# Optimization experiments

Measured on AMD Instinct MI355X. Metric: run time of the kernel, lower is better.

The kernel has to match this reference:

```python
import jax, jax.numpy as jnp
import numpy as np

B, Q, K, DQ, DK = 4, 256, 1024, 256, 256


def setup_inputs() -> dict:
    key = jax.random.key(0)
    ks = jax.random.split(key, 7)
    q = jax.random.normal(ks[0], (B, Q, DQ), dtype=jnp.float32)
    k = jax.random.normal(ks[1], (B, K, DK), dtype=jnp.float32)
    v = jax.random.normal(ks[2], (B, K, DK), dtype=jnp.float32)
    mask = jax.random.randint(ks[3], (B, K), 0, 2).astype(bool)
    # torch Linear(in,out,bias=False): y = x @ W.T ; store as [in,out] for einsum
    Wq = jax.random.normal(ks[4], (DQ, DK), dtype=jnp.float32) / np.sqrt(DQ)
    Wk = jax.random.normal(ks[5], (DK, DK), dtype=jnp.float32) / np.sqrt(DK)
    wv = jax.random.normal(ks[6], (DK,), dtype=jnp.float32) / np.sqrt(DK)
    return {"q": q, "k": k, "v": v, "mask": mask, "Wq": Wq, "Wk": Wk, "wv": wv}


def reference(q, k, v, mask, Wq, Wk, wv):
    # Additive (Bahdanau) attention. Original redundantly projects repeated
    # copies; projecting once then broadcasting is the same math.
    qp = jnp.einsum('bqd,de->bqe', q, Wq)          # [B,Q,DK]
    kp = jnp.einsum('bkd,de->bke', k, Wk)          # [B,K,DK]
    h = jnp.tanh(qp[:, :, None, :] + kp[:, None, :, :])  # [B,Q,K,DK]
    scores = jnp.einsum('bqke,e->bqk', h, wv)      # [B,Q,K]
    scores = jnp.where(mask[:, None, :], scores, -jnp.inf)
    probs = jax.nn.softmax(scores, axis=-1)        # [B,Q,K]
    attended = jnp.einsum('bqk,bkd->bqd', probs, v)
    return attended
```

## Files before the change

kernel.cpp:

```cpp
#include <hip/hip_runtime.h>
#include <hip/hip_bf16.h>

#define B_ 4
#define Q_ 256
#define K_ 1024
#define D_ 256
#define LOG2E 1.44269504f

__device__ __forceinline__ float fexp2(float x) {
    float r; asm("v_exp_f32 %0, %1" : "=v"(r) : "v"(x)); return r;
}
__device__ __forceinline__ float frcp(float x) {
    float r; asm("v_rcp_f32 %0, %1" : "=v"(r) : "v"(x)); return r;
}
__device__ __forceinline__ void gload_lds16(const void* g, void* l) {
    __builtin_amdgcn_global_load_lds((const __attribute__((address_space(1))) void*)g,
                                     (__attribute__((address_space(3))) void*)l, 16, 0, 0);
}

__global__ __launch_bounds__(256) void prep_kernel(const float* __restrict__ q,
                                                   const float* __restrict__ k,
                                                   const float* __restrict__ Wq,
                                                   const float* __restrict__ Wk,
                                                   const int* __restrict__ mask,
                                                   float* __restrict__ qpE,
                                                   float* __restrict__ kpE,
                                                   ushort* __restrict__ kidx,
                                                   int* __restrict__ nvalid,
                                                   float scale) {
    const int t = threadIdx.x;
    if (blockIdx.x >= 80) {
        if (t >= 64) return;
        const int b = blockIdx.y, lane = t;
        const int* m = mask + b * K_;
        const int base = lane * 16;
        int cnt = 0;
#pragma unroll
        for (int i = 0; i < 16; ++i) cnt += (m[base + i] != 0);
        int inc = cnt;
#pragma unroll
        for (int d = 1; d < 64; d <<= 1) {
            int tt = __shfl_up(inc, d);
            if (lane >= d) inc += tt;
        }
        const int total = __shfl(inc, 63);
        int pos = inc - cnt;
        ushort* kb = kidx + b * K_;
        for (int i = 0; i < 16; ++i) {
            int kk = base + i;
            if (m[kk] != 0) kb[pos++] = (ushort)kk;
        }
        for (int j = total + lane; j < K_; j += 64) kb[j] = 0;
        if (lane == 0) nvalid[b] = total;
        return;
    }
    const float* A; const float* W; float* outp; int m0;
    if (blockIdx.x < 16) { A = q; W = Wq; outp = qpE; m0 = blockIdx.x * 64; }
    else                 { A = k; W = Wk; outp = kpE; m0 = (blockIdx.x - 16) * 64; }
    __shared__ float As[16][65];
    __shared__ float Ws[16][64];
    const int tx = t & 15, ty = t >> 4;
    const int n0 = blockIdx.y * 64;
    const int ar = t >> 2, ac = (t & 3) * 4;
    const int wr = t >> 4, wc = (t & 15) * 4;
    float c[4][4] = {};
    for (int kb = 0; kb < 256; kb += 16) {
        __syncthreads();
        float4 av = *(const float4*)(A + (size_t)(m0 + ar) * 256 + kb + ac);
        As[ac + 0][ar] = av.x; As[ac + 1][ar] = av.y;
        As[ac + 2][ar] = av.z; As[ac + 3][ar] = av.w;
        float4 wvv = *(const float4*)(W + (size_t)(kb + wr) * 256 + n0 + wc);
        wvv.x *= scale; wvv.y *= scale; wvv.z *= scale; wvv.w *= scale;
        *(float4*)(&Ws[wr][wc]) = wvv;
        __syncthreads();
#pragma unroll
        for (int kk = 0; kk < 16; ++kk) {
            float4 bv = *(const float4*)(&Ws[kk][tx * 4]);
#pragma unroll
            for (int i = 0; i < 4; ++i) {
                float a = As[kk][ty * 4 + i];
                c[i][0] = fmaf(a, bv.x, c[i][0]);
                c[i][1] = fmaf(a, bv.y, c[i][1]);
                c[i][2] = fmaf(a, bv.z, c[i][2]);
                c[i][3] = fmaf(a, bv.w, c[i][3]);
            }
        }
    }
#pragma unroll
    for (int i = 0; i < 4; ++i) {
        float4 o = make_float4(fexp2(c[i][0]), fexp2(c[i][1]),
                               fexp2(c[i][2]), fexp2(c[i][3]));
        *(float4*)(outp + (size_t)(m0 + ty * 4 + i) * 256 + n0 + tx * 4) = o;
    }
}

__global__ __launch_bounds__(1024, 2) void attn_kernel(const float* __restrict__ qpE,
                                                       const float* __restrict__ kpE,
                                                       const float* __restrict__ v,
                                                       const ushort* __restrict__ kidx_g,
                                                       const int* __restrict__ nvalid_g,
                                                       const float* __restrict__ wv,
                                                       float* __restrict__ out) {
    __shared__ float4 s_kp[2][32 * 65];
    __shared__ float  s_red[16 * 66];
    __shared__ float  s_sc[2][1024];
    __shared__ ushort s_kidx[1024];
    __shared__ float  s_inv[2];

    const int tid  = threadIdx.x;
    const int lane = tid & 63;
    const int wave = tid >> 6;
    const int kl   = lane & 31;
    const int eh   = lane >> 5;

    int bid = blockIdx.x;
    bid = (bid & 7) * 64 + (bid >> 3);
    const int b  = bid >> 7;
    const int qi = bid & 127;
    const int q0 = qi * 2;

    const int nv     = nvalid_g[b];
    const int ntiles = (nv + 31) >> 5;
    const int ntot   = ntiles << 5;

    s_kidx[tid] = (tid < nv) ? kidx_g[b * K_ + tid] : (ushort)0;

    float qp_A[2][8], wv_r[8];
    {
        const int e0 = wave * 16 + eh * 8;
#pragma unroll
        for (int qq = 0; qq < 2; ++qq) {
            const float4* p = (const float4*)(qpE + ((size_t)(b * Q_ + q0 + qq) << 8) + e0);
#pragma unroll
            for (int i = 0; i < 2; ++i) {
                float4 x = p[i];
                qp_A[qq][i * 4 + 0] = x.x; qp_A[qq][i * 4 + 1] = x.y;
                qp_A[qq][i * 4 + 2] = x.z; qp_A[qq][i * 4 + 3] = x.w;
            }
        }
        const float4* pw = (const float4*)(wv + e0);
#pragma unroll
        for (int i = 0; i < 2; ++i) {
            float4 x = pw[i];
            wv_r[i * 4 + 0] = x.x; wv_r[i * 4 + 1] = x.y;
            wv_r[i * 4 + 2] = x.z; wv_r[i * 4 + 3] = x.w;
        }
    }
    __syncthreads();

    const float4* srcb = (const float4*)(kpE + ((size_t)b * K_ << 8));

    if (ntiles > 0) {
#pragma unroll
        for (int i = 0; i < 2; ++i) {
            const int row = wave * 2 + i;
            const int gr = s_kidx[row];
            gload_lds16(srcb + ((size_t)gr << 6) + lane, &s_kp[0][row * 65]);
        }
    }
    __syncthreads();

    for (int kt = 0; kt < ntiles; ++kt) {
        const int p = kt & 1;
        if (kt + 1 < ntiles) {
            const int o = (kt + 1) * 32;
#pragma unroll
            for (int i = 0; i < 2; ++i) {
                const int row = wave * 2 + i;
                const int gr = s_kidx[o + row];
                gload_lds16(srcb + ((size_t)gr << 6) + lane, &s_kp[p ^ 1][row * 65]);
            }
        }
        float a0 = 0.f, a1 = 0.f;
        const float4* krow = s_kp[p] + kl * 65 + wave * 4 + eh * 2;
#pragma unroll
        for (int t4 = 0; t4 < 2; ++t4) {
            float4 kv = krow[t4];
            float kc[4] = {kv.x, kv.y, kv.z, kv.w};
#pragma unroll
            for (int j = 0; j < 4; ++j) {
                const int e = t4 * 4 + j;
                const float w = wv_r[e];
                float r0 = frcp(fmaf(qp_A[0][e], kc[j], 1.0f));
                a0 = fmaf(w, r0, a0);
                float r1 = frcp(fmaf(qp_A[1][e], kc[j], 1.0f));
                a1 = fmaf(w, r1, a1);
            }
        }
        a0 += __shfl_xor(a0, 32);
        a1 += __shfl_xor(a1, 32);
        if (eh == 0) {
            s_red[wave * 66 + kl]      = a0;
            s_red[wave * 66 + 32 + kl] = a1;
        }
        __syncthreads();

        {
            const int w = tid & 15, sl = tid >> 4;
            float s = s_red[w * 66 + sl];
            s += __shfl_xor(s, 1);
            s += __shfl_xor(s, 2);
            s += __shfl_xor(s, 4);
            s += __shfl_xor(s, 8);
            if (w == 0) {
                const int idx = kt * 32 + (sl & 31);
                s_sc[sl >> 5][idx] = (idx < nv) ? (-2.0f * s) : -3.0e38f;
            }
        }
        __syncthreads();
    }

    if (wave < 2) {
        const int qq = wave;
        float mx = -3.0e38f;
        for (int j = lane; j < ntot; j += 64) mx = fmaxf(mx, s_sc[qq][j]);
#pragma unroll
        for (int off = 32; off > 0; off >>= 1) mx = fmaxf(mx, __shfl_xor(mx, off));
        float sum = 0.f;
        for (int j = lane; j < ntot; j += 64) {
            float e = fexp2((s_sc[qq][j] - mx) * LOG2E);
            s_sc[qq][j] = e;
            sum += e;
        }
#pragma unroll
        for (int off = 32; off > 0; off >>= 1) sum += __shfl_xor(sum, off);
        if (lane == 0) s_inv[qq] = frcp(sum);
    }
    __syncthreads();

    {
        const int dl = tid & 63;
        const int kq = tid >> 6;
        const int chunk = ntiles * 2;
        float4 o0 = {0, 0, 0, 0}, o1 = {0, 0, 0, 0};
        const float4* v4 = (const float4*)(v + ((size_t)b * K_ << 8));
        for (int k = kq * chunk; k < kq * chunk + chunk; ++k) {
            int vr = s_kidx[k];
            float4 vv = v4[((size_t)vr << 6) + dl];
            float p0 = s_sc[0][k], p1 = s_sc[1][k];
            o0.x = fmaf(p0, vv.x, o0.x); o0.y = fmaf(p0, vv.y, o0.y);
            o0.z = fmaf(p0, vv.z, o0.z); o0.w = fmaf(p0, vv.w, o0.w);
            o1.x = fmaf(p1, vv.x, o1.x); o1.y = fmaf(p1, vv.y, o1.y);
            o1.z = fmaf(p1, vv.z, o1.z); o1.w = fmaf(p1, vv.w, o1.w);
        }
        float4* s_pv = s_kp[0];
        s_pv[(kq * 2 + 0) * 64 + dl] = o0;
        s_pv[(kq * 2 + 1) * 64 + dl] = o1;
        __syncthreads();
        if (tid < 128) {
            const int qq = tid >> 6, c = tid & 63;
            float4 s = {0, 0, 0, 0};
#pragma unroll
            for (int g = 0; g < 16; ++g) {
                float4 x = s_pv[(g * 2 + qq) * 64 + c];
                s.x += x.x; s.y += x.y; s.z += x.z; s.w += x.w;
            }
            const float inv = s_inv[qq];
            s.x *= inv; s.y *= inv; s.z *= inv; s.w *= inv;
            ((float4*)out)[((size_t)(b * Q_ + q0 + qq) << 6) + c] = s;
        }
    }
}

extern "C" void kernel_launch(void* const* d_in, const int* in_sizes, int n_in,
                              void* d_out, int out_size, void* d_ws, size_t ws_size,
                              hipStream_t stream) {
    const float* q    = (const float*)d_in[0];
    const float* k    = (const float*)d_in[1];
    const float* v    = (const float*)d_in[2];
    const int*   mask = (const int*)d_in[3];
    const float* Wq   = (const float*)d_in[4];
    const float* Wk   = (const float*)d_in[5];
    const float* wv   = (const float*)d_in[6];
    float* out = (float*)d_out;

    float* qpE    = (float*)d_ws;
    float* kpE    = qpE + (size_t)B_ * Q_ * D_;
    ushort* kidx  = (ushort*)(kpE + (size_t)B_ * K_ * D_);
    int* nvalid   = (int*)(kidx + (size_t)B_ * K_);

    const float c2 = 2.885390082f;

    prep_kernel<<<dim3(81, 4), 256, 0, stream>>>(q, k, Wq, Wk, mask, qpE, kpE, kidx, nvalid, c2);
    attn_kernel<<<dim3(512), 1024, 0, stream>>>(qpE, kpE, v, kidx, nvalid, wv, out);
}
```

Measured before the change: 65.71 us.

## Assign one key per thread for scores, dropping tiled LDS staging and reductions

The score phase changes from a tiled scheme, where 16 waves split the feature dimension over 32-key tiles staged in LDS with global_load_lds and reduced through shuffles plus two barriers per tile, to a scheme where each thread computes a full 256-wide dot product for one key. The key rows are read straight from global memory and qp and wv are broadcast from LDS. The block size drops to 512 threads with launch bounds (512,4), and the PV loop strides over valid keys instead of padded tiles. This removes the per-tile barriers and cross-wave reductions, but each thread now reads a separate 1 KB key row, so the loads are uncoalesced and served mostly by L1/L2. It also relies on about 512 valid keys per batch for load balance.

```diff
diff --git a/kernel.cpp b/kernel.cpp
--- a/kernel.cpp
+++ b/kernel.cpp
@@ -12,10 +12,6 @@
 }
 __device__ __forceinline__ float frcp(float x) {
     float r; asm("v_rcp_f32 %0, %1" : "=v"(r) : "v"(x)); return r;
-}
-__device__ __forceinline__ void gload_lds16(const void* g, void* l) {
-    __builtin_amdgcn_global_load_lds((const __attribute__((address_space(1))) void*)g,
-                                     (__attribute__((address_space(3))) void*)l, 16, 0, 0);
 }
 
 __global__ __launch_bounds__(256) void prep_kernel(const float* __restrict__ q,
@@ -94,24 +90,21 @@
     }
 }
 
-__global__ __launch_bounds__(1024, 2) void attn_kernel(const float* __restrict__ qpE,
-                                                       const float* __restrict__ kpE,
-                                                       const float* __restrict__ v,
-                                                       const ushort* __restrict__ kidx_g,
-                                                       const int* __restrict__ nvalid_g,
-                                                       const float* __restrict__ wv,
-                                                       float* __restrict__ out) {
-    __shared__ float4 s_kp[2][32 * 65];
-    __shared__ float  s_red[16 * 66];
+__global__ __launch_bounds__(512, 4) void attn_kernel(const float* __restrict__ qpE,
+                                                      const float* __restrict__ kpE,
+                                                      const float* __restrict__ v,
+                                                      const ushort* __restrict__ kidx_g,
+                                                      const int* __restrict__ nvalid_g,
+                                                      const float* __restrict__ wv,
+                                                      float* __restrict__ out) {
+    __shared__ float  s_qpA[2][256];
+    __shared__ float  s_wv[256];
+    __shared__ ushort s_kidx[1024];
     __shared__ float  s_sc[2][1024];
-    __shared__ ushort s_kidx[1024];
+    __shared__ float4 s_pv[16][64];
     __shared__ float  s_inv[2];
 
-    const int tid  = threadIdx.x;
-    const int lane = tid & 63;
-    const int wave = tid >> 6;
-    const int kl   = lane & 31;
-    const int eh   = lane >> 5;
+    const int tid = threadIdx.x;
 
     int bid = blockIdx.x;
     bid = (bid & 7) * 64 + (bid >> 3);
@@ -119,105 +112,52 @@
     const int qi = bid & 127;
     const int q0 = qi * 2;
 
-    const int nv     = nvalid_g[b];
-    const int ntiles = (nv + 31) >> 5;
-    const int ntot   = ntiles << 5;
-
-    s_kidx[tid] = (tid < nv) ? kidx_g[b * K_ + tid] : (ushort)0;
-
-    float qp_A[2][8], wv_r[8];
-    {
-        const int e0 = wave * 16 + eh * 8;
-#pragma unroll
-        for (int qq = 0; qq < 2; ++qq) {
-            const float4* p = (const float4*)(qpE + ((size_t)(b * Q_ + q0 + qq) << 8) + e0);
-#pragma unroll
-            for (int i = 0; i < 2; ++i) {
-                float4 x = p[i];
-                qp_A[qq][i * 4 + 0] = x.x; qp_A[qq][i * 4 + 1] = x.y;
-                qp_A[qq][i * 4 + 2] = x.z; qp_A[qq][i * 4 + 3] = x.w;
-            }
-        }
-        const float4* pw = (const float4*)(wv + e0);
-#pragma unroll
-        for (int i = 0; i < 2; ++i) {
-            float4 x = pw[i];
-            wv_r[i * 4 + 0] = x.x; wv_r[i * 4 + 1] = x.y;
-            wv_r[i * 4 + 2] = x.z; wv_r[i * 4 + 3] = x.w;
-        }
-    }
+    const int nv = nvalid_g[b];
+
+    if (tid < 64)        ((float4*)s_qpA[0])[tid]      = ((const float4*)(qpE + ((size_t)(b * Q_ + q0)     << 8)))[tid];
+    else if (tid < 128)  ((float4*)s_qpA[1])[tid - 64] = ((const float4*)(qpE + ((size_t)(b * Q_ + q0 + 1) << 8)))[tid - 64];
+    else if (tid < 192)  ((float4*)s_wv)[tid - 128]    = ((const float4*)wv)[tid - 128];
+    s_kidx[tid]       = (tid < nv)       ? kidx_g[b * K_ + tid]       : (ushort)0;
+    s_kidx[tid + 512] = (tid + 512 < nv) ? kidx_g[b * K_ + tid + 512] : (ushort)0;
     __syncthreads();
 
-    const float4* srcb = (const float4*)(kpE + ((size_t)b * K_ << 8));
-
-    if (ntiles > 0) {
-#pragma unroll
-        for (int i = 0; i < 2; ++i) {
-            const int row = wave * 2 + i;
-            const int gr = s_kidx[row];
-            gload_lds16(srcb + ((size_t)gr << 6) + lane, &s_kp[0][row * 65]);
-        }
+    for (int slot = tid; slot < nv; slot += 512) {
+        const int kk = s_kidx[slot];
+        const float4* kr = (const float4*)(kpE + (((size_t)(b * K_ + kk)) << 8));
+        const float4* A0p = (const float4*)s_qpA[0];
+        const float4* A1p = (const float4*)s_qpA[1];
+        const float4* Wp  = (const float4*)s_wv;
+        float a0 = 0.f, a1 = 0.f;
+#pragma unroll 4
+        for (int e4 = 0; e4 < 64; ++e4) {
+            float4 Bv = kr[e4];
+            float4 A0 = A0p[e4];
+            float4 A1 = A1p[e4];
+            float4 W4 = Wp[e4];
+            a0 = fmaf(W4.x, frcp(fmaf(A0.x, Bv.x, 1.f)), a0);
+            a1 = fmaf(W4.x, frcp(fmaf(A1.x, Bv.x, 1.f)), a1);
+            a0 = fmaf(W4.y, frcp(fmaf(A0.y, Bv.y, 1.f)), a0);
+            a1 = fmaf(W4.y, frcp(fmaf(A1.y, Bv.y, 1.f)), a1);
+            a0 = fmaf(W4.z, frcp(fmaf(A0.z, Bv.z, 1.f)), a0);
+            a1 = fmaf(W4.z, frcp(fmaf(A1.z, Bv.z, 1.f)), a1);
+            a0 = fmaf(W4.w, frcp(fmaf(A0.w, Bv.w, 1.f)), a0);
+            a1 = fmaf(W4.w, frcp(fmaf(A1.w, Bv.w, 1.f)), a1);
+        }
+        s_sc[0][slot] = -2.f * a0;
+        s_sc[1][slot] = -2.f * a1;
     }
     __syncthreads();
 
-    for (int kt = 0; kt < ntiles; ++kt) {
-        const int p = kt & 1;
-        if (kt + 1 < ntiles) {
-            const int o = (kt + 1) * 32;
-#pragma unroll
-            for (int i = 0; i < 2; ++i) {
-                const int row = wave * 2 + i;
-                const int gr = s_kidx[o + row];
-                gload_lds16(srcb + ((size_t)gr << 6) + lane, &s_kp[p ^ 1][row * 65]);
-            }
-        }
-        float a0 = 0.f, a1 = 0.f;
-        const float4* krow = s_kp[p] + kl * 65 + wave * 4 + eh * 2;
-#pragma unroll
-        for (int t4 = 0; t4 < 2; ++t4) {
-            float4 kv = krow[t4];
-            float kc[4] = {kv.x, kv.y, kv.z, kv.w};
-#pragma unroll
-            for (int j = 0; j < 4; ++j) {
-                const int e = t4 * 4 + j;
-                const float w = wv_r[e];
-                float r0 = frcp(fmaf(qp_A[0][e], kc[j], 1.0f));
-                a0 = fmaf(w, r0, a0);
-                float r1 = frcp(fmaf(qp_A[1][e], kc[j], 1.0f));
-                a1 = fmaf(w, r1, a1);
-            }
-        }
-        a0 += __shfl_xor(a0, 32);
-        a1 += __shfl_xor(a1, 32);
-        if (eh == 0) {
-            s_red[wave * 66 + kl]      = a0;
-            s_red[wave * 66 + 32 + kl] = a1;
-        }
-        __syncthreads();
-
-        {
-            const int w = tid & 15, sl = tid >> 4;
-            float s = s_red[w * 66 + sl];
-            s += __shfl_xor(s, 1);
-            s += __shfl_xor(s, 2);
-            s += __shfl_xor(s, 4);
-            s += __shfl_xor(s, 8);
-            if (w == 0) {
-                const int idx = kt * 32 + (sl & 31);
-                s_sc[sl >> 5][idx] = (idx < nv) ? (-2.0f * s) : -3.0e38f;
-            }
-        }
-        __syncthreads();
-    }
-
+    const int lane = tid & 63;
+    const int wave = tid >> 6;
     if (wave < 2) {
         const int qq = wave;
         float mx = -3.0e38f;
-        for (int j = lane; j < ntot; j += 64) mx = fmaxf(mx, s_sc[qq][j]);
+        for (int j = lane; j < nv; j += 64) mx = fmaxf(mx, s_sc[qq][j]);
 #pragma unroll
         for (int off = 32; off > 0; off >>= 1) mx = fmaxf(mx, __shfl_xor(mx, off));
         float sum = 0.f;
-        for (int j = lane; j < ntot; j += 64) {
+        for (int j = lane; j < nv; j += 64) {
             float e = fexp2((s_sc[qq][j] - mx) * LOG2E);
             s_sc[qq][j] = e;
             sum += e;
@@ -231,10 +171,9 @@
     {
         const int dl = tid & 63;
         const int kq = tid >> 6;
-        const int chunk = ntiles * 2;
         float4 o0 = {0, 0, 0, 0}, o1 = {0, 0, 0, 0};
         const float4* v4 = (const float4*)(v + ((size_t)b * K_ << 8));
-        for (int k = kq * chunk; k < kq * chunk + chunk; ++k) {
+        for (int k = kq; k < nv; k += 8) {
             int vr = s_kidx[k];
             float4 vv = v4[((size_t)vr << 6) + dl];
             float p0 = s_sc[0][k], p1 = s_sc[1][k];
@@ -243,16 +182,15 @@
             o1.x = fmaf(p1, vv.x, o1.x); o1.y = fmaf(p1, vv.y, o1.y);
             o1.z = fmaf(p1, vv.z, o1.z); o1.w = fmaf(p1, vv.w, o1.w);
         }
-        float4* s_pv = s_kp[0];
-        s_pv[(kq * 2 + 0) * 64 + dl] = o0;
-        s_pv[(kq * 2 + 1) * 64 + dl] = o1;
+        s_pv[kq * 2 + 0][dl] = o0;
+        s_pv[kq * 2 + 1][dl] = o1;
         __syncthreads();
         if (tid < 128) {
             const int qq = tid >> 6, c = tid & 63;
             float4 s = {0, 0, 0, 0};
 #pragma unroll
-            for (int g = 0; g < 16; ++g) {
-                float4 x = s_pv[(g * 2 + qq) * 64 + c];
+            for (int g = 0; g < 8; ++g) {
+                float4 x = s_pv[g * 2 + qq][c];
                 s.x += x.x; s.y += x.y; s.z += x.z; s.w += x.w;
             }
             const float inv = s_inv[qq];
@@ -282,5 +220,5 @@
     const float c2 = 2.885390082f;
 
     prep_kernel<<<dim3(81, 4), 256, 0, stream>>>(q, k, Wq, Wk, mask, qpE, kpE, kidx, nvalid, c2);
-    attn_kernel<<<dim3(512), 1024, 0, stream>>>(qpE, kpE, v, kidx, nvalid, wv, out);
-}
+    attn_kernel<<<dim3(512), 512, 0, stream>>>(qpE, kpE, v, kidx, nvalid, wv, out);
+}
```

Result: slower. 75.55 us (+15.0%).
